# Kernel tuning notes

Measured on AMD Instinct MI355X. Metric: run time of the kernel, lower is better.

## Reference

```python
import jax, jax.numpy as jnp
import numpy as np

NUM_HEADS = 8
SCALE = 0.125  # 1/sqrt(head_dim=64)
NEG_INF = -1e30
LN_EPS = 1e-5


def _layer_norm(x, gamma, beta):
    m = jnp.mean(x, axis=-1, keepdims=True)
    v = jnp.mean(jnp.square(x - m), axis=-1, keepdims=True)
    return (x - m) * jax.lax.rsqrt(v + LN_EPS) * gamma + beta


def setup_inputs() -> dict:
    key = jax.random.key(0)
    ks = jax.random.split(key, 12)
    B, Q, K, D = 2, 2048, 2048, 512
    inp = {
        "query": jax.random.normal(ks[0], (B, Q, D), jnp.float32),
        "key": jax.random.normal(ks[1], (B, K, D), jnp.float32),
        "value": jax.random.normal(ks[2], (B, K, D), jnp.float32),
        "weight_q": jax.random.normal(ks[3], (D, D), jnp.float32) * (1.0 / np.sqrt(D)),
        "weight_k": jax.random.normal(ks[4], (D, D), jnp.float32) * (1.0 / np.sqrt(D)),
        "weight_v": jax.random.normal(ks[5], (D, D), jnp.float32) * (1.0 / np.sqrt(D)),
        "weight_o": jax.random.normal(ks[6], (D, D), jnp.float32) * (1.0 / np.sqrt(D)),
        "g_w": jax.random.normal(ks[7], (2 * D, D), jnp.float32) * (1.0 / np.sqrt(2 * D)),
        "g_b": jnp.ones((D,), jnp.float32),  # g_net bias init to 1.0
        "q_gamma": jnp.ones((D,), jnp.float32),
        "q_beta": jnp.zeros((D,), jnp.float32),
        "k_gamma": jnp.ones((D,), jnp.float32),
        "k_beta": jnp.zeros((D,), jnp.float32),
        "v_gamma": jnp.ones((D,), jnp.float32),
        "v_beta": jnp.zeros((D,), jnp.float32),
        "query_mask": jax.random.randint(ks[8], (B, Q), 0, 2, jnp.int32),
        "key_mask": jax.random.randint(ks[9], (B, K), 0, 2, jnp.int32),
    }
    return inp


def reference(query, key, value, weight_q, weight_k, weight_v, weight_o,
              g_w, g_b, q_gamma, q_beta, k_gamma, k_beta, v_gamma, v_beta,
              query_mask, key_mask):
    B, Q, D = query.shape
    H = NUM_HEADS
    original_query = query

    # add_zero_attn: append an all-zero key/value slot (mask bit = 1)
    key = jnp.concatenate([key, jnp.zeros((B, 1, key.shape[-1]), key.dtype)], axis=1)
    value = jnp.concatenate([value, jnp.zeros((B, 1, value.shape[-1]), value.dtype)], axis=1)
    km = jnp.concatenate([key_mask, jnp.ones((B, 1), key_mask.dtype)], axis=1)
    Kp = key.shape[1]  # klen + 1

    # pre_lnorm
    qn = _layer_norm(query, q_gamma, q_beta)
    kn = _layer_norm(key, k_gamma, k_beta)
    vn = _layer_norm(value, v_gamma, v_beta)

    # multi-head dot-product scores: [B, Q, Kp, H]
    qh = (qn @ weight_q).reshape(B, Q, H, -1)
    kh = (kn @ weight_k).reshape(B, Kp, H, -1)
    score = jnp.einsum('bind,bjnd->bijn', qh, kh) * SCALE
    score = jnp.where(km[:, None, :, None] == 0, NEG_INF, score)
    attn = jax.nn.softmax(score, axis=2)  # softmax over klen (dim=2)

    # weighted values
    vh = (vn @ weight_v).reshape(B, Kp, H, -1)
    attn_vec = jnp.einsum('bijn,bjnd->bind', attn, vh).reshape(B, Q, -1)

    # query mask zeroing
    attn_vec = jnp.where(query_mask[:, :, None] == 0, jnp.zeros((), attn_vec.dtype), attn_vec)

    # output projection
    attn_vec = attn_vec @ weight_o

    # gated combination
    g = jax.nn.sigmoid(jnp.concatenate([original_query, attn_vec], axis=-1) @ g_w + g_b)
    attn_out = g * original_query + (1.0 - g) * attn_vec

    # residual
    attn_out = original_query + attn_out
    return attn_out
```

## Files before the change

kernel.cpp:

```cpp
#include <hip/hip_runtime.h>

typedef float f32x4 __attribute__((ext_vector_type(4)));
typedef short s16x8 __attribute__((ext_vector_type(8)));

#define DEV __device__ __forceinline__

DEV short f2bf(float f) {
    union { float f; unsigned u; } v; v.f = f;
    unsigned r = v.u + 0x7fffu + ((v.u >> 16) & 1u);
    return (short)(r >> 16);
}
DEV float bf2f(short s) {
    union { unsigned u; float f; } v; v.u = ((unsigned)(unsigned short)s) << 16;
    return v.f;
}

#define SEQ    2048
#define DMODEL 512
#define KPAD   2080
#define NROWS  32768

#define OFF_QN   0ull
#define OFF_KN   4194304ull
#define OFF_VN   8519680ull
#define OFF_QH   12845056ull
#define OFF_KH   17039360ull
#define OFF_VH   21364736ull
#define OFF_VHT  25690112ull
#define OFF_AV   29949952ull
#define OFF_WQT  34144256ull
#define WS_NEEDED 37289984ull
#define OFF_ON   0ull
#define OFF_ML   21364736ull
#define OFF_KB   29949952ull
#define OFF_AP   17039360ull

__global__ __launch_bounds__(256) void ln_all(
    const float* __restrict__ q, const float* __restrict__ k, const float* __restrict__ v,
    const float* __restrict__ qg, const float* __restrict__ qb,
    const float* __restrict__ kg, const float* __restrict__ kb2,
    const float* __restrict__ vg, const float* __restrict__ vb,
    short* __restrict__ qn, short* __restrict__ kn, short* __restrict__ vn)
{
    int bid = blockIdx.x;
    const float *in, *gamma, *beta; short* out; int Sreal, Spad;
    if (bid < 1024)      { in=q; gamma=qg; beta=qb;  out=qn; Sreal=SEQ; Spad=SEQ;  }
    else if (bid < 2080) { bid-=1024; in=k; gamma=kg; beta=kb2; out=kn; Sreal=SEQ; Spad=KPAD; }
    else                 { bid-=2080; in=v; gamma=vg; beta=vb;  out=vn; Sreal=SEQ; Spad=KPAD; }

    int w = threadIdx.x >> 6, l = threadIdx.x & 63;
    int r = bid * 4 + w;
    short* op = out + (size_t)r * DMODEL + l * 8;
    s16x8 o = {0,0,0,0,0,0,0,0};
    if (r >= 2 * Spad) { *(s16x8*)op = o; return; }
    int b = r / Spad, j = r - b * Spad;
    if (j >= Sreal) {
        if (j == Sreal) {
            f32x4 b0 = *(const f32x4*)(beta + l*8);
            f32x4 b1 = *(const f32x4*)(beta + l*8 + 4);
            #pragma unroll
            for (int t=0;t<4;t++){ o[t]=f2bf(b0[t]); o[t+4]=f2bf(b1[t]); }
        }
        *(s16x8*)op = o; return;
    }
    const float* ip = in + ((size_t)b * Sreal + j) * DMODEL + l * 8;
    f32x4 x0 = *(const f32x4*)ip;
    f32x4 x1 = *(const f32x4*)(ip + 4);
    float s = x0[0]+x0[1]+x0[2]+x0[3]+x1[0]+x1[1]+x1[2]+x1[3];
    #pragma unroll
    for (int off=1; off<64; off<<=1) s += __shfl_xor(s, off);
    float mean = s * (1.0f/512.0f);
    float vs = 0.f;
    #pragma unroll
    for (int t=0;t<4;t++){ float d0=x0[t]-mean, d1=x1[t]-mean; vs += d0*d0 + d1*d1; }
    #pragma unroll
    for (int off=1; off<64; off<<=1) vs += __shfl_xor(vs, off);
    float rstd = rsqrtf(vs * (1.0f/512.0f) + 1e-5f);
    f32x4 g0 = *(const f32x4*)(gamma + l*8), g1 = *(const f32x4*)(gamma + l*8 + 4);
    f32x4 b0 = *(const f32x4*)(beta + l*8),  b1 = *(const f32x4*)(beta + l*8 + 4);
    #pragma unroll
    for (int t=0;t<4;t++){
        o[t]   = f2bf((x0[t]-mean)*rstd*g0[t] + b0[t]);
        o[t+4] = f2bf((x1[t]-mean)*rstd*g1[t] + b1[t]);
    }
    *(s16x8*)op = o;
}

__global__ __launch_bounds__(256) void wt_all(
    const float* __restrict__ Wq, const float* __restrict__ Wk,
    const float* __restrict__ Wv, const float* __restrict__ Wo,
    const float* __restrict__ gW, short* __restrict__ WT,
    const int* __restrict__ km, float* __restrict__ kbias)
{
    int bid = blockIdx.x;
    if (bid >= 1536) {
        int i = (bid - 1536) * 256 + threadIdx.x;
        if (i >= 2 * KPAD) return;
        int b = i / KPAD, j = i - b * KPAD;
        float v;
        if (j < SEQ)       v = km[b*SEQ + j] ? 0.0f : -1e30f;
        else if (j == SEQ) v = 0.0f;
        else               v = -1e30f;
        kbias[i] = v;
        return;
    }
    const float* in; short* out; int K;
    if (bid < 1024) {
        int wsel = bid >> 8;
        in = (wsel==0) ? Wq : (wsel==1) ? Wk : (wsel==2) ? Wv : Wo;
        out = WT + (size_t)wsel * 262144;
        K = 512; bid &= 255;
    } else {
        in = gW; out = WT + 1048576; K = 1024; bid -= 1024;
    }
    __shared__ float t[32][33];
    int bx = bid & 15, by = bid >> 4;
    int n0 = bx * 32, k0 = by * 32;
    int tx = threadIdx.x & 31, ty = threadIdx.x >> 5;
    #pragma unroll
    for (int i=0;i<4;i++)
        t[ty + i*8][tx] = in[(size_t)(k0 + ty + i*8) * 512 + n0 + tx];
    __syncthreads();
    #pragma unroll
    for (int i=0;i<4;i++)
        out[(size_t)(n0 + ty + i*8) * K + k0 + tx] = f2bf(t[tx][ty + i*8]);
}

template<int MODE, int KK>
__global__ __launch_bounds__(256) void gemm_u(
    const short* __restrict__ A, const float* __restrict__ F1, const float* __restrict__ F2,
    const short* __restrict__ WT,
    short* __restrict__ O0, short* __restrict__ O1, short* __restrict__ O2,
    float* __restrict__ FO, const float* __restrict__ bias)
{
    __shared__ short As[128*64];
    __shared__ short Bs[64*64];
    int tid = threadIdx.x;
    int w = tid >> 6, l = tid & 63;
    int lr = l & 15, lg = l >> 4;
    int tn = blockIdx.x & 7, tm = blockIdx.x >> 3;
    int srow = tid >> 3, sslot = tid & 7;

    const short* Bseg = WT;
    if (MODE == 0) {
        int seg = (tm < 32) ? 0 : (tm < 65) ? 1 : 2;
        Bseg = WT + (size_t)seg * 262144;
    }

    f32x4 acc[2][4];
    #pragma unroll
    for (int m=0;m<2;m++)
        #pragma unroll
        for (int n=0;n<4;n++) acc[m][n] = (f32x4){0.f,0.f,0.f,0.f};

    for (int k0 = 0; k0 < KK; k0 += 64) {
        #pragma unroll
        for (int i=0;i<2;i++){
            int row = i*32 + srow;
            int gslot = sslot ^ (row & 7);
            const short* gb = Bseg + (size_t)(tn*64 + row) * KK + k0 + gslot*8;
            short* lb = Bs + (i*256 + w*64) * 8;
            __builtin_amdgcn_global_load_lds((const __attribute__((address_space(1))) void*)gb,
                                             (__attribute__((address_space(3))) void*)lb, 16, 0, 0);
        }
        if (MODE != 2) {
            #pragma unroll
            for (int i=0;i<4;i++){
                int row = i*32 + srow;
                int gslot = sslot ^ (row & 7);
                const short* ga = A + (size_t)(tm*128 + row) * KK + k0 + gslot*8;
                short* la = As + (i*256 + w*64) * 8;
                __builtin_amdgcn_global_load_lds((const __attribute__((address_space(1))) void*)ga,
                                                 (__attribute__((address_space(3))) void*)la, 16, 0, 0);
            }
        } else {
            const float* src = (k0 < 512) ? F1 : F2;
            int csub = (k0 < 512) ? k0 : k0 - 512;
            #pragma unroll
            for (int i=0;i<4;i++){
                int row = i*32 + srow;
                const float* gp = src + (size_t)(tm*128 + row) * 512 + csub + sslot*8;
                f32x4 a0 = *(const f32x4*)gp;
                f32x4 a1 = *(const f32x4*)(gp + 4);
                s16x8 o;
                #pragma unroll
                for (int t=0;t<4;t++){ o[t] = f2bf(a0[t]); o[t+4] = f2bf(a1[t]); }
                *(s16x8*)(As + row*64 + (sslot ^ (row & 7))*8) = o;
            }
        }
        __syncthreads();
        #pragma unroll
        for (int s=0;s<2;s++){
            s16x8 af[2], bfr[4];
            #pragma unroll
            for (int m=0;m<2;m++){
                int row = w*32 + m*16 + lr;
                int slot = (s*4 + lg) ^ (row & 7);
                af[m] = *(const s16x8*)(As + row*64 + slot*8);
            }
            #pragma unroll
            for (int n=0;n<4;n++){
                int row = n*16 + lr;
                int slot = (s*4 + lg) ^ (row & 7);
                bfr[n] = *(const s16x8*)(Bs + row*64 + slot*8);
            }
            #pragma unroll
            for (int m=0;m<2;m++)
                #pragma unroll
                for (int n=0;n<4;n++)
                    acc[m][n] = __builtin_amdgcn_mfma_f32_16x16x32_bf16(af[m], bfr[n], acc[m][n], 0, 0, 0);
        }
        __syncthreads();
    }

    #pragma unroll
    for (int n=0;n<4;n++){
        int col = tn*64 + n*16 + lr;
        float badd = (MODE == 2) ? bias[col] : 0.0f;
        #pragma unroll
        for (int m=0;m<2;m++){
            #pragma unroll
            for (int j=0;j<4;j++){
                int row = tm*128 + w*32 + m*16 + lg*4 + j;
                float v = acc[m][n][j];
                if (MODE == 0) {
                    short bv = f2bf(v);
                    if (row < 4096) {
                        O0[(size_t)row*512 + col] = bv;
                    } else if (row < 8320) {
                        int r2 = row - 4096;
                        if (r2 < 4160) O1[(size_t)r2*512 + col] = bv;
                    } else {
                        int r2 = row - 8320;
                        if (r2 < 4160) O2[(size_t)r2*512 + col] = bv;
                    }
                } else if (MODE == 1) {
                    FO[(size_t)row*512 + col] = v;
                } else {
                    size_t idx = (size_t)row*512 + col;
                    float g = 1.0f / (1.0f + __expf(-(v + badd)));
                    float q = F1[idx], a = F2[idx];
                    FO[idx] = q + g*q + (1.0f - g)*a;
                }
            }
        }
    }
}

__global__ __launch_bounds__(256) void transpose_v(
    const short* __restrict__ vh, short* __restrict__ vhT)
{
    __shared__ short t[64][72];
    int tid = threadIdx.x, bid = blockIdx.x;
    int kt = bid % 33; int hh = (bid / 33) & 7; int b = bid / (33*8);
    int k0 = kt * 64;
    int rr = tid >> 3, c8 = (tid & 7) * 8;
    #pragma unroll
    for (int p=0;p<2;p++){
        int kr = p*32 + rr;
        int gk = k0 + kr;
        s16x8 v = {0,0,0,0,0,0,0,0};
        if (gk < KPAD) v = *(const s16x8*)(vh + (size_t)(b*KPAD + gk)*DMODEL + hh*64 + c8);
        *(s16x8*)&t[kr][c8] = v;
    }
    __syncthreads();
    #pragma unroll
    for (int p=0;p<2;p++){
        int dr = p*32 + rr;
        if (k0 + c8 < KPAD){
            s16x8 o;
            #pragma unroll
            for (int j2=0;j2<8;j2++) o[j2] = t[c8+j2][dr];
            *(s16x8*)(vhT + ((size_t)(b*8 + hh)*64 + dr)*KPAD + k0 + c8) = o;
        }
    }
}

__global__ __launch_bounds__(256, 6) void flash_kernel(
    const short* __restrict__ qh, const short* __restrict__ kh,
    const short* __restrict__ vhT, const float* __restrict__ kbias,
    short* __restrict__ On, float* __restrict__ ml)
{
    __shared__ short Ks[64*64];
    __shared__ short Vs[64*64];
    __shared__ short plds[4][16*72];
    int tid = threadIdx.x;
    int w = tid >> 6, l = tid & 63;
    int bid = blockIdx.x;
    int h = bid & 7;
    int b = (bid >> 3) & 1;
    int t = bid >> 4;
    int qblk = t / 3;
    int split = t - qblk * 3;
    int q0 = qblk * 64 + w * 16;
    int cl = l & 15, rg = l >> 4;
    int srow = tid >> 3, sslot = tid & 7;

    const short* qp = qh + ((size_t)(b*SEQ + q0 + cl))*DMODEL + h*64 + rg*8;
    s16x8 qf0 = *(const s16x8*)qp;
    s16x8 qf1 = *(const s16x8*)(qp + 32);

    f32x4 O[4];
    float mrow[4], lsum[4];
    #pragma unroll
    for (int n=0;n<4;n++) O[n] = (f32x4){0.f,0.f,0.f,0.f};
    #pragma unroll
    for (int j=0;j<4;j++){ mrow[j] = -1e30f; lsum[j] = 0.f; }

    const short* khb = kh + (size_t)b*KPAD*DMODEL + h*64;
    const short* vtb = vhT + (size_t)(b*8 + h)*64*KPAD;
    const float* kbb = kbias + b*KPAD;
    short* pl = plds[w];

    int kc0 = split * 11;
    int kcN = kc0 + ((split == 2) ? 10 : 11);
    for (int kc = kc0; kc < kcN; ++kc) {
        int k0 = kc * 64;
        if (kc > kc0) __syncthreads();
        #pragma unroll
        for (int i=0;i<2;i++){
            int row = i*32 + srow;
            int gslot = sslot ^ (row & 7);
            const short* gk = khb + (size_t)(k0 + row)*DMODEL + gslot*8;
            const short* gv = vtb + (size_t)row*KPAD + k0 + gslot*8;
            short* lk = Ks + (i*256 + w*64)*8;
            short* lv = Vs + (i*256 + w*64)*8;
            __builtin_amdgcn_global_load_lds((const __attribute__((address_space(1))) void*)gk,
                                             (__attribute__((address_space(3))) void*)lk, 16, 0, 0);
            __builtin_amdgcn_global_load_lds((const __attribute__((address_space(1))) void*)gv,
                                             (__attribute__((address_space(3))) void*)lv, 16, 0, 0);
        }
        __syncthreads();

        float sv[4][4];
        #pragma unroll
        for (int nh=0; nh<4; ++nh) {
            int row = nh*16 + cl;
            s16x8 ka  = *(const s16x8*)(Ks + row*64 + ((rg)     ^ (row & 7))*8);
            s16x8 kb2 = *(const s16x8*)(Ks + row*64 + ((4 + rg) ^ (row & 7))*8);
            f32x4 z = (f32x4){0.f,0.f,0.f,0.f};
            z = __builtin_amdgcn_mfma_f32_16x16x32_bf16(qf0, ka,  z, 0, 0, 0);
            z = __builtin_amdgcn_mfma_f32_16x16x32_bf16(qf1, kb2, z, 0, 0, 0);
            float bias = kbb[k0 + nh*16 + cl];
            #pragma unroll
            for (int j=0;j<4;j++) sv[nh][j] = fmaf(z[j], 0.125f, bias);
        }
        float ml4[4];
        #pragma unroll
        for (int j=0;j<4;j++)
            ml4[j] = fmaxf(fmaxf(sv[0][j], sv[1][j]), fmaxf(sv[2][j], sv[3][j]));
        #pragma unroll
        for (int off=1; off<16; off<<=1){
            #pragma unroll
            for (int j=0;j<4;j++) ml4[j] = fmaxf(ml4[j], __shfl_xor(ml4[j], off));
        }
        bool need = (ml4[0] > mrow[0]+8.f) || (ml4[1] > mrow[1]+8.f) ||
                    (ml4[2] > mrow[2]+8.f) || (ml4[3] > mrow[3]+8.f);
        if (__any(need)) {
            #pragma unroll
            for (int j=0;j<4;j++){
                float mn = fmaxf(mrow[j], ml4[j]);
                float sc = __expf(mrow[j] - mn);
                mrow[j] = mn; lsum[j] *= sc;
                #pragma unroll
                for (int n=0;n<4;n++) O[n][j] *= sc;
            }
        }
        float ps[4] = {0.f,0.f,0.f,0.f};
        #pragma unroll
        for (int nh=0; nh<4; ++nh){
            #pragma unroll
            for (int j=0;j<4;j++){
                float p = __expf(sv[nh][j] - mrow[j]);
                ps[j] += p;
                pl[(rg*4 + j)*72 + nh*16 + cl] = f2bf(p);
            }
        }
        #pragma unroll
        for (int off=1; off<16; off<<=1){
            #pragma unroll
            for (int j=0;j<4;j++) ps[j] += __shfl_xor(ps[j], off);
        }
        #pragma unroll
        for (int j=0;j<4;j++) lsum[j] += ps[j];

        s16x8 pa0 = *(const s16x8*)(pl + cl*72 + rg*8);
        s16x8 pa1 = *(const s16x8*)(pl + cl*72 + 32 + rg*8);
        __builtin_amdgcn_s_setprio(1);
        #pragma unroll
        for (int n=0;n<4;n++){
            int row = n*16 + cl;
            s16x8 vf0 = *(const s16x8*)(Vs + row*64 + ((rg)     ^ (row & 7))*8);
            s16x8 vf1 = *(const s16x8*)(Vs + row*64 + ((4 + rg) ^ (row & 7))*8);
            O[n] = __builtin_amdgcn_mfma_f32_16x16x32_bf16(pa0, vf0, O[n], 0, 0, 0);
            O[n] = __builtin_amdgcn_mfma_f32_16x16x32_bf16(pa1, vf1, O[n], 0, 0, 0);
        }
        __builtin_amdgcn_s_setprio(0);
    }

    if (split == 2) {
        int k0 = 2048;
        float sv[2][4];
        #pragma unroll
        for (int nh=0; nh<2; ++nh) {
            const short* kp = khb + (size_t)(k0 + nh*16 + cl)*DMODEL + rg*8;
            s16x8 ka = *(const s16x8*)kp;
            s16x8 kb2 = *(const s16x8*)(kp + 32);
            f32x4 z = (f32x4){0.f,0.f,0.f,0.f};
            z = __builtin_amdgcn_mfma_f32_16x16x32_bf16(qf0, ka,  z, 0, 0, 0);
            z = __builtin_amdgcn_mfma_f32_16x16x32_bf16(qf1, kb2, z, 0, 0, 0);
            float bias = kbb[k0 + nh*16 + cl];
            #pragma unroll
            for (int j=0;j<4;j++) sv[nh][j] = fmaf(z[j], 0.125f, bias);
        }
        float ml4[4];
        #pragma unroll
        for (int j=0;j<4;j++) ml4[j] = fmaxf(sv[0][j], sv[1][j]);
        #pragma unroll
        for (int off=1; off<16; off<<=1){
            #pragma unroll
            for (int j=0;j<4;j++) ml4[j] = fmaxf(ml4[j], __shfl_xor(ml4[j], off));
        }
        bool need = (ml4[0] > mrow[0]+8.f) || (ml4[1] > mrow[1]+8.f) ||
                    (ml4[2] > mrow[2]+8.f) || (ml4[3] > mrow[3]+8.f);
        if (__any(need)) {
            #pragma unroll
            for (int j=0;j<4;j++){
                float mn = fmaxf(mrow[j], ml4[j]);
                float sc = __expf(mrow[j] - mn);
                mrow[j] = mn; lsum[j] *= sc;
                #pragma unroll
                for (int n=0;n<4;n++) O[n][j] *= sc;
            }
        }
        float ps[4] = {0.f,0.f,0.f,0.f};
        #pragma unroll
        for (int nh=0; nh<2; ++nh){
            #pragma unroll
            for (int j=0;j<4;j++){
                float p = __expf(sv[nh][j] - mrow[j]);
                ps[j] += p;
                pl[(rg*4 + j)*72 + nh*16 + cl] = f2bf(p);
            }
        }
        #pragma unroll
        for (int off=1; off<16; off<<=1){
            #pragma unroll
            for (int j=0;j<4;j++) ps[j] += __shfl_xor(ps[j], off);
        }
        #pragma unroll
        for (int j=0;j<4;j++) lsum[j] += ps[j];

        s16x8 pa0 = *(const s16x8*)(pl + cl*72 + rg*8);
        __builtin_amdgcn_s_setprio(1);
        #pragma unroll
        for (int n=0;n<4;n++){
            s16x8 vf0 = *(const s16x8*)(vtb + (size_t)(n*16 + cl)*KPAD + k0 + rg*8);
            O[n] = __builtin_amdgcn_mfma_f32_16x16x32_bf16(pa0, vf0, O[n], 0, 0, 0);
        }
        __builtin_amdgcn_s_setprio(0);
    }

    int rbase = ((b*8 + h) << 11) + q0;
    #pragma unroll
    for (int j=0;j<4;j++){
        int r = rbase + rg*4 + j;
        float invl = 1.0f / lsum[j];
        #pragma unroll
        for (int n=0;n<4;n++)
            On[((size_t)split*NROWS + r)*64 + n*16 + cl] = f2bf(O[n][j] * invl);
        if (cl == 0){
            ml[((size_t)split*NROWS + r)*2    ] = mrow[j];
            ml[((size_t)split*NROWS + r)*2 + 1] = lsum[j];
        }
    }
}

__global__ __launch_bounds__(256) void merge_kernel(
    const short* __restrict__ On, const float* __restrict__ ml,
    const int* __restrict__ qmask, short* __restrict__ av)
{
    int tid = threadIdx.x;
    int r = blockIdx.x * 32 + (tid >> 3);
    int d8 = (tid & 7) * 8;
    float m0 = ml[(size_t)r*2],              l0 = ml[(size_t)r*2 + 1];
    float m1 = ml[((size_t)NROWS + r)*2],    l1 = ml[((size_t)NROWS + r)*2 + 1];
    float m2 = ml[((size_t)2*NROWS + r)*2],  l2 = ml[((size_t)2*NROWS + r)*2 + 1];
    float m = fmaxf(m0, fmaxf(m1, m2));
    float w0 = l0 * __expf(m0 - m), w1 = l1 * __expf(m1 - m), w2 = l2 * __expf(m2 - m);
    int qrow = r & 2047, bh = r >> 11, h = bh & 7, b = bh >> 3;
    int qm = qmask[b*SEQ + qrow];
    float inv = qm ? 1.0f / (w0 + w1 + w2) : 0.0f;
    w0 *= inv; w1 *= inv; w2 *= inv;
    s16x8 o0 = *(const s16x8*)(On + (size_t)r*64 + d8);
    s16x8 o1 = *(const s16x8*)(On + ((size_t)NROWS + r)*64 + d8);
    s16x8 o2 = *(const s16x8*)(On + ((size_t)2*NROWS + r)*64 + d8);
    s16x8 o;
    #pragma unroll
    for (int e=0;e<8;e++) o[e] = f2bf(w0*bf2f(o0[e]) + w1*bf2f(o1[e]) + w2*bf2f(o2[e]));
    *(s16x8*)(av + ((size_t)(b*SEQ + qrow))*DMODEL + h*64 + d8) = o;
}

extern "C" void kernel_launch(void* const* d_in, const int* in_sizes, int n_in,
                              void* d_out, int out_size, void* d_ws, size_t ws_size,
                              hipStream_t stream)
{
    const float* query = (const float*)d_in[0];
    const float* key   = (const float*)d_in[1];
    const float* value = (const float*)d_in[2];
    const float* Wq    = (const float*)d_in[3];
    const float* Wk    = (const float*)d_in[4];
    const float* Wv    = (const float*)d_in[5];
    const float* Wo    = (const float*)d_in[6];
    const float* gW    = (const float*)d_in[7];
    const float* gB    = (const float*)d_in[8];
    const float* qg    = (const float*)d_in[9];
    const float* qb    = (const float*)d_in[10];
    const float* kg    = (const float*)d_in[11];
    const float* kb    = (const float*)d_in[12];
    const float* vg    = (const float*)d_in[13];
    const float* vb    = (const float*)d_in[14];
    const int* qmask   = (const int*)d_in[15];
    const int* kmask   = (const int*)d_in[16];
    float* out = (float*)d_out;
    char* ws = (char*)d_ws;

    if (ws_size < WS_NEEDED) return;

    short* qn  = (short*)(ws + OFF_QN);
    short* kn  = (short*)(ws + OFF_KN);
    short* vn  = (short*)(ws + OFF_VN);
    short* qh  = (short*)(ws + OFF_QH);
    short* khp = (short*)(ws + OFF_KH);
    short* vhp = (short*)(ws + OFF_VH);
    short* vhT = (short*)(ws + OFF_VHT);
    short* av  = (short*)(ws + OFF_AV);
    short* WT  = (short*)(ws + OFF_WQT);
    short* WoT = WT + 3*262144;
    short* gWT = WT + 1048576;
    short* On  = (short*)(ws + OFF_ON);
    float* mlp = (float*)(ws + OFF_ML);
    float* kbp = (float*)(ws + OFF_KB);
    float* ap  = (float*)(ws + OFF_AP);

    ln_all<<<3136, 256, 0, stream>>>(query, key, value, qg, qb, kg, kb, vg, vb, qn, kn, vn);

    wt_all<<<1553, 256, 0, stream>>>(Wq, Wk, Wv, Wo, gW, WT, kmask, kbp);

    gemm_u<0,512><<<784, 256, 0, stream>>>(qn, nullptr, nullptr, WT, qh, khp, vhp, nullptr, nullptr);

    transpose_v<<<528, 256, 0, stream>>>(vhp, vhT);

    flash_kernel<<<1536, 256, 0, stream>>>(qh, khp, vhT, kbp, On, mlp);
    merge_kernel<<<1024, 256, 0, stream>>>(On, mlp, qmask, av);

    gemm_u<1,512><<<256, 256, 0, stream>>>(av, nullptr, nullptr, WoT, nullptr, nullptr, nullptr, ap, nullptr);

    gemm_u<2,1024><<<256, 256, 0, stream>>>(nullptr, query, ap, gWT, nullptr, nullptr, nullptr, out, gB);

    (void)in_sizes; (void)n_in; (void)out_size;
}
```

Measured before the change: 240.2 us.

## Fuse prep kernels, fold split-merge into output GEMM, shrink GEMM tiles to 64x64

The layernorm and weight-transpose/key-bias kernels are merged into one launch, and padding rows shrink (KPAD rows trimmed to 2064 blocks). The split-K flash merge is folded into the Wo GEMM's A-tile loader, which drops a kernel launch and the intermediate av buffer round-trip. GEMM tiles go from 128x64 to 64x64 with a 2x2 wave layout, doubling the grid for better CU occupancy. The cost is recomputing the merge weights per k-block in the GEMM and smaller MFMA reuse per block.

Result: faster. 231.4 us (-3.7%).

```diff
diff --git a/kernel.cpp b/kernel.cpp
--- a/kernel.cpp
+++ b/kernel.cpp
@@ -22,86 +22,83 @@
 
 #define OFF_QN   0ull
 #define OFF_KN   4194304ull
-#define OFF_VN   8519680ull
+#define OFF_VN   8454144ull
 #define OFF_QH   12845056ull
 #define OFF_KH   17039360ull
 #define OFF_VH   21364736ull
 #define OFF_VHT  25690112ull
-#define OFF_AV   29949952ull
+#define OFF_KB   29949952ull
+#define OFF_ML   29966592ull
 #define OFF_WQT  34144256ull
 #define WS_NEEDED 37289984ull
 #define OFF_ON   0ull
-#define OFF_ML   21364736ull
-#define OFF_KB   29949952ull
 #define OFF_AP   17039360ull
 
-__global__ __launch_bounds__(256) void ln_all(
+__global__ __launch_bounds__(256) void prep_all(
     const float* __restrict__ q, const float* __restrict__ k, const float* __restrict__ v,
     const float* __restrict__ qg, const float* __restrict__ qb,
     const float* __restrict__ kg, const float* __restrict__ kb2,
     const float* __restrict__ vg, const float* __restrict__ vb,
-    short* __restrict__ qn, short* __restrict__ kn, short* __restrict__ vn)
+    const float* __restrict__ Wq, const float* __restrict__ Wk,
+    const float* __restrict__ Wv, const float* __restrict__ Wo,
+    const float* __restrict__ gW, const int* __restrict__ km,
+    short* __restrict__ qn, short* __restrict__ kn, short* __restrict__ vn,
+    short* __restrict__ WT, float* __restrict__ kbias)
 {
     int bid = blockIdx.x;
-    const float *in, *gamma, *beta; short* out; int Sreal, Spad;
-    if (bid < 1024)      { in=q; gamma=qg; beta=qb;  out=qn; Sreal=SEQ; Spad=SEQ;  }
-    else if (bid < 2080) { bid-=1024; in=k; gamma=kg; beta=kb2; out=kn; Sreal=SEQ; Spad=KPAD; }
-    else                 { bid-=2080; in=v; gamma=vg; beta=vb;  out=vn; Sreal=SEQ; Spad=KPAD; }
-
-    int w = threadIdx.x >> 6, l = threadIdx.x & 63;
-    int r = bid * 4 + w;
-    short* op = out + (size_t)r * DMODEL + l * 8;
-    s16x8 o = {0,0,0,0,0,0,0,0};
-    if (r >= 2 * Spad) { *(s16x8*)op = o; return; }
-    int b = r / Spad, j = r - b * Spad;
-    if (j >= Sreal) {
-        if (j == Sreal) {
-            f32x4 b0 = *(const f32x4*)(beta + l*8);
-            f32x4 b1 = *(const f32x4*)(beta + l*8 + 4);
-            #pragma unroll
-            for (int t=0;t<4;t++){ o[t]=f2bf(b0[t]); o[t+4]=f2bf(b1[t]); }
-        }
-        *(s16x8*)op = o; return;
-    }
-    const float* ip = in + ((size_t)b * Sreal + j) * DMODEL + l * 8;
-    f32x4 x0 = *(const f32x4*)ip;
-    f32x4 x1 = *(const f32x4*)(ip + 4);
-    float s = x0[0]+x0[1]+x0[2]+x0[3]+x1[0]+x1[1]+x1[2]+x1[3];
-    #pragma unroll
-    for (int off=1; off<64; off<<=1) s += __shfl_xor(s, off);
-    float mean = s * (1.0f/512.0f);
-    float vs = 0.f;
-    #pragma unroll
-    for (int t=0;t<4;t++){ float d0=x0[t]-mean, d1=x1[t]-mean; vs += d0*d0 + d1*d1; }
-    #pragma unroll
-    for (int off=1; off<64; off<<=1) vs += __shfl_xor(vs, off);
-    float rstd = rsqrtf(vs * (1.0f/512.0f) + 1e-5f);
-    f32x4 g0 = *(const f32x4*)(gamma + l*8), g1 = *(const f32x4*)(gamma + l*8 + 4);
-    f32x4 b0 = *(const f32x4*)(beta + l*8),  b1 = *(const f32x4*)(beta + l*8 + 4);
-    #pragma unroll
-    for (int t=0;t<4;t++){
-        o[t]   = f2bf((x0[t]-mean)*rstd*g0[t] + b0[t]);
-        o[t+4] = f2bf((x1[t]-mean)*rstd*g1[t] + b1[t]);
-    }
-    *(s16x8*)op = o;
-}
-
-__global__ __launch_bounds__(256) void wt_all(
-    const float* __restrict__ Wq, const float* __restrict__ Wk,
-    const float* __restrict__ Wv, const float* __restrict__ Wo,
-    const float* __restrict__ gW, short* __restrict__ WT,
-    const int* __restrict__ km, float* __restrict__ kbias)
-{
-    int bid = blockIdx.x;
+    if (bid < 3104) {
+        const float *in, *gamma, *beta; short* out; int Spad;
+        if (bid < 1024)      { in=q; gamma=qg; beta=qb;  out=qn; Spad=SEQ;  }
+        else if (bid < 2064) { bid-=1024; in=k; gamma=kg; beta=kb2; out=kn; Spad=KPAD; }
+        else                 { bid-=2064; in=v; gamma=vg; beta=vb;  out=vn; Spad=KPAD; }
+
+        int w = threadIdx.x >> 6, l = threadIdx.x & 63;
+        int r = bid * 4 + w;
+        short* op = out + (size_t)r * DMODEL + l * 8;
+        s16x8 o = {0,0,0,0,0,0,0,0};
+        int b = r / Spad, j = r - b * Spad;
+        if (j >= SEQ) {
+            if (j == SEQ) {
+                f32x4 b0 = *(const f32x4*)(beta + l*8);
+                f32x4 b1 = *(const f32x4*)(beta + l*8 + 4);
+                #pragma unroll
+                for (int t=0;t<4;t++){ o[t]=f2bf(b0[t]); o[t+4]=f2bf(b1[t]); }
+            }
+            *(s16x8*)op = o; return;
+        }
+        const float* ip = in + ((size_t)b * SEQ + j) * DMODEL + l * 8;
+        f32x4 x0 = *(const f32x4*)ip;
+        f32x4 x1 = *(const f32x4*)(ip + 4);
+        float s = x0[0]+x0[1]+x0[2]+x0[3]+x1[0]+x1[1]+x1[2]+x1[3];
+        #pragma unroll
+        for (int off=1; off<64; off<<=1) s += __shfl_xor(s, off);
+        float mean = s * (1.0f/512.0f);
+        float vs = 0.f;
+        #pragma unroll
+        for (int t=0;t<4;t++){ float d0=x0[t]-mean, d1=x1[t]-mean; vs += d0*d0 + d1*d1; }
+        #pragma unroll
+        for (int off=1; off<64; off<<=1) vs += __shfl_xor(vs, off);
+        float rstd = rsqrtf(vs * (1.0f/512.0f) + 1e-5f);
+        f32x4 g0 = *(const f32x4*)(gamma + l*8), g1 = *(const f32x4*)(gamma + l*8 + 4);
+        f32x4 b0 = *(const f32x4*)(beta + l*8),  b1 = *(const f32x4*)(beta + l*8 + 4);
+        #pragma unroll
+        for (int t=0;t<4;t++){
+            o[t]   = f2bf((x0[t]-mean)*rstd*g0[t] + b0[t]);
+            o[t+4] = f2bf((x1[t]-mean)*rstd*g1[t] + b1[t]);
+        }
+        *(s16x8*)op = o;
+        return;
+    }
+    bid -= 3104;
     if (bid >= 1536) {
         int i = (bid - 1536) * 256 + threadIdx.x;
         if (i >= 2 * KPAD) return;
         int b = i / KPAD, j = i - b * KPAD;
-        float v;
-        if (j < SEQ)       v = km[b*SEQ + j] ? 0.0f : -1e30f;
-        else if (j == SEQ) v = 0.0f;
-        else               v = -1e30f;
-        kbias[i] = v;
+        float val;
+        if (j < SEQ)       val = km[b*SEQ + j] ? 0.0f : -1e30f;
+        else if (j == SEQ) val = 0.0f;
+        else               val = -1e30f;
+        kbias[i] = val;
         return;
     }
     const float* in; short* out; int K;
@@ -127,31 +124,33 @@
 }
 
 template<int MODE, int KK>
-__global__ __launch_bounds__(256) void gemm_u(
+__global__ __launch_bounds__(256) void gemm64(
     const short* __restrict__ A, const float* __restrict__ F1, const float* __restrict__ F2,
     const short* __restrict__ WT,
     short* __restrict__ O0, short* __restrict__ O1, short* __restrict__ O2,
-    float* __restrict__ FO, const float* __restrict__ bias)
+    float* __restrict__ FO, const float* __restrict__ bias,
+    const short* __restrict__ On, const float* __restrict__ mlp, const int* __restrict__ qmask)
 {
-    __shared__ short As[128*64];
+    __shared__ short As[64*64];
     __shared__ short Bs[64*64];
     int tid = threadIdx.x;
     int w = tid >> 6, l = tid & 63;
     int lr = l & 15, lg = l >> 4;
-    int tn = blockIdx.x & 7, tm = blockIdx.x >> 3;
+    int tm = blockIdx.x >> 3, tn = blockIdx.x & 7;
+    int wm = w >> 1, wn = w & 1;
     int srow = tid >> 3, sslot = tid & 7;
 
     const short* Bseg = WT;
     if (MODE == 0) {
-        int seg = (tm < 32) ? 0 : (tm < 65) ? 1 : 2;
+        int seg = (tm < 64) ? 0 : (tm < 129) ? 1 : 2;
         Bseg = WT + (size_t)seg * 262144;
     }
 
-    f32x4 acc[2][4];
+    f32x4 acc[2][2];
     #pragma unroll
     for (int m=0;m<2;m++)
         #pragma unroll
-        for (int n=0;n<4;n++) acc[m][n] = (f32x4){0.f,0.f,0.f,0.f};
+        for (int n=0;n<2;n++) acc[m][n] = (f32x4){0.f,0.f,0.f,0.f};
 
     for (int k0 = 0; k0 < KK; k0 += 64) {
         #pragma unroll
@@ -163,23 +162,46 @@
             __builtin_amdgcn_global_load_lds((const __attribute__((address_space(1))) void*)gb,
                                              (__attribute__((address_space(3))) void*)lb, 16, 0, 0);
         }
-        if (MODE != 2) {
-            #pragma unroll
-            for (int i=0;i<4;i++){
+        if (MODE == 0) {
+            #pragma unroll
+            for (int i=0;i<2;i++){
                 int row = i*32 + srow;
                 int gslot = sslot ^ (row & 7);
-                const short* ga = A + (size_t)(tm*128 + row) * KK + k0 + gslot*8;
+                const short* ga = A + (size_t)(tm*64 + row) * KK + k0 + gslot*8;
                 short* la = As + (i*256 + w*64) * 8;
                 __builtin_amdgcn_global_load_lds((const __attribute__((address_space(1))) void*)ga,
                                                  (__attribute__((address_space(3))) void*)la, 16, 0, 0);
             }
+        } else if (MODE == 1) {
+            int h = k0 >> 6;
+            #pragma unroll
+            for (int i=0;i<2;i++){
+                int row = i*32 + srow;
+                int r = tm*64 + row;
+                int b = r >> 11, qrow = r & 2047;
+                int rr = ((b*8 + h) << 11) + qrow;
+                float m0 = mlp[(size_t)rr*2],               l0 = mlp[(size_t)rr*2 + 1];
+                float m1 = mlp[((size_t)NROWS + rr)*2],     l1 = mlp[((size_t)NROWS + rr)*2 + 1];
+                float m2 = mlp[((size_t)2*NROWS + rr)*2],   l2 = mlp[((size_t)2*NROWS + rr)*2 + 1];
+                float mm = fmaxf(m0, fmaxf(m1, m2));
+                float w0 = l0 * __expf(m0 - mm), w1 = l1 * __expf(m1 - mm), w2 = l2 * __expf(m2 - mm);
+                float inv = qmask[b*SEQ + qrow] ? 1.0f / (w0 + w1 + w2) : 0.0f;
+                w0 *= inv; w1 *= inv; w2 *= inv;
+                s16x8 o0 = *(const s16x8*)(On + ((size_t)rr)*64 + sslot*8);
+                s16x8 o1 = *(const s16x8*)(On + ((size_t)NROWS + rr)*64 + sslot*8);
+                s16x8 o2 = *(const s16x8*)(On + ((size_t)2*NROWS + rr)*64 + sslot*8);
+                s16x8 om;
+                #pragma unroll
+                for (int e=0;e<8;e++) om[e] = f2bf(w0*bf2f(o0[e]) + w1*bf2f(o1[e]) + w2*bf2f(o2[e]));
+                *(s16x8*)(As + row*64 + (sslot ^ (row & 7))*8) = om;
+            }
         } else {
             const float* src = (k0 < 512) ? F1 : F2;
             int csub = (k0 < 512) ? k0 : k0 - 512;
             #pragma unroll
-            for (int i=0;i<4;i++){
+            for (int i=0;i<2;i++){
                 int row = i*32 + srow;
-                const float* gp = src + (size_t)(tm*128 + row) * 512 + csub + sslot*8;
+                const float* gp = src + (size_t)(tm*64 + row) * 512 + csub + sslot*8;
                 f32x4 a0 = *(const f32x4*)gp;
                 f32x4 a1 = *(const f32x4*)(gp + 4);
                 s16x8 o;
@@ -191,56 +213,50 @@
         __syncthreads();
         #pragma unroll
         for (int s=0;s<2;s++){
-            s16x8 af[2], bfr[4];
+            s16x8 af[2], bfr[2];
             #pragma unroll
             for (int m=0;m<2;m++){
-                int row = w*32 + m*16 + lr;
+                int row = wm*32 + m*16 + lr;
                 int slot = (s*4 + lg) ^ (row & 7);
                 af[m] = *(const s16x8*)(As + row*64 + slot*8);
             }
             #pragma unroll
-            for (int n=0;n<4;n++){
-                int row = n*16 + lr;
+            for (int n=0;n<2;n++){
+                int row = wn*32 + n*16 + lr;
                 int slot = (s*4 + lg) ^ (row & 7);
                 bfr[n] = *(const s16x8*)(Bs + row*64 + slot*8);
             }
             #pragma unroll
             for (int m=0;m<2;m++)
                 #pragma unroll
-                for (int n=0;n<4;n++)
+                for (int n=0;n<2;n++)
                     acc[m][n] = __builtin_amdgcn_mfma_f32_16x16x32_bf16(af[m], bfr[n], acc[m][n], 0, 0, 0);
         }
         __syncthreads();
     }
 
     #pragma unroll
-    for (int n=0;n<4;n++){
-        int col = tn*64 + n*16 + lr;
+    for (int n=0;n<2;n++){
+        int col = tn*64 + wn*32 + n*16 + lr;
         float badd = (MODE == 2) ? bias[col] : 0.0f;
         #pragma unroll
         for (int m=0;m<2;m++){
             #pragma unroll
             for (int j=0;j<4;j++){
-                int row = tm*128 + w*32 + m*16 + lg*4 + j;
+                int row = tm*64 + wm*32 + m*16 + lg*4 + j;
                 float v = acc[m][n][j];
                 if (MODE == 0) {
                     short bv = f2bf(v);
-                    if (row < 4096) {
-                        O0[(size_t)row*512 + col] = bv;
-                    } else if (row < 8320) {
-                        int r2 = row - 4096;
-                        if (r2 < 4160) O1[(size_t)r2*512 + col] = bv;
-                    } else {
-                        int r2 = row - 8320;
-                        if (r2 < 4160) O2[(size_t)r2*512 + col] = bv;
-                    }
+                    if (row < 4096)      O0[(size_t)row*512 + col] = bv;
+                    else if (row < 8256) O1[(size_t)(row - 4096)*512 + col] = bv;
+                    else                 O2[(size_t)(row - 8256)*512 + col] = bv;
                 } else if (MODE == 1) {
                     FO[(size_t)row*512 + col] = v;
                 } else {
                     size_t idx = (size_t)row*512 + col;
                     float g = 1.0f / (1.0f + __expf(-(v + badd)));
-                    float q = F1[idx], a = F2[idx];
-                    FO[idx] = q + g*q + (1.0f - g)*a;
+                    float qv = F1[idx], a = F2[idx];
+                    FO[idx] = qv + g*qv + (1.0f - g)*a;
                 }
             }
         }
@@ -474,31 +490,6 @@
             ml[((size_t)split*NROWS + r)*2 + 1] = lsum[j];
         }
     }
-}
-
-__global__ __launch_bounds__(256) void merge_kernel(
-    const short* __restrict__ On, const float* __restrict__ ml,
-    const int* __restrict__ qmask, short* __restrict__ av)
-{
-    int tid = threadIdx.x;
-    int r = blockIdx.x * 32 + (tid >> 3);
-    int d8 = (tid & 7) * 8;
-    float m0 = ml[(size_t)r*2],              l0 = ml[(size_t)r*2 + 1];
-    float m1 = ml[((size_t)NROWS + r)*2],    l1 = ml[((size_t)NROWS + r)*2 + 1];
-    float m2 = ml[((size_t)2*NROWS + r)*2],  l2 = ml[((size_t)2*NROWS + r)*2 + 1];
-    float m = fmaxf(m0, fmaxf(m1, m2));
-    float w0 = l0 * __expf(m0 - m), w1 = l1 * __expf(m1 - m), w2 = l2 * __expf(m2 - m);
-    int qrow = r & 2047, bh = r >> 11, h = bh & 7, b = bh >> 3;
-    int qm = qmask[b*SEQ + qrow];
-    float inv = qm ? 1.0f / (w0 + w1 + w2) : 0.0f;
-    w0 *= inv; w1 *= inv; w2 *= inv;
-    s16x8 o0 = *(const s16x8*)(On + (size_t)r*64 + d8);
-    s16x8 o1 = *(const s16x8*)(On + ((size_t)NROWS + r)*64 + d8);
-    s16x8 o2 = *(const s16x8*)(On + ((size_t)2*NROWS + r)*64 + d8);
-    s16x8 o;
-    #pragma unroll
-    for (int e=0;e<8;e++) o[e] = f2bf(w0*bf2f(o0[e]) + w1*bf2f(o1[e]) + w2*bf2f(o2[e]));
-    *(s16x8*)(av + ((size_t)(b*SEQ + qrow))*DMODEL + h*64 + d8) = o;
 }
 
 extern "C" void kernel_launch(void* const* d_in, const int* in_sizes, int n_in,
@@ -534,7 +525,6 @@
     short* khp = (short*)(ws + OFF_KH);
     short* vhp = (short*)(ws + OFF_VH);
     short* vhT = (short*)(ws + OFF_VHT);
-    short* av  = (short*)(ws + OFF_AV);
     short* WT  = (short*)(ws + OFF_WQT);
     short* WoT = WT + 3*262144;
     short* gWT = WT + 1048576;
@@ -543,20 +533,22 @@
     float* kbp = (float*)(ws + OFF_KB);
     float* ap  = (float*)(ws + OFF_AP);
 
-    ln_all<<<3136, 256, 0, stream>>>(query, key, value, qg, qb, kg, kb, vg, vb, qn, kn, vn);
-
-    wt_all<<<1553, 256, 0, stream>>>(Wq, Wk, Wv, Wo, gW, WT, kmask, kbp);
-
-    gemm_u<0,512><<<784, 256, 0, stream>>>(qn, nullptr, nullptr, WT, qh, khp, vhp, nullptr, nullptr);
+    prep_all<<<4657, 256, 0, stream>>>(query, key, value, qg, qb, kg, kb, vg, vb,
+                                       Wq, Wk, Wv, Wo, gW, kmask,
+                                       qn, kn, vn, WT, kbp);
+
+    gemm64<0,512><<<1552, 256, 0, stream>>>(qn, nullptr, nullptr, WT, qh, khp, vhp,
+                                            nullptr, nullptr, nullptr, nullptr, nullptr);
 
     transpose_v<<<528, 256, 0, stream>>>(vhp, vhT);
 
     flash_kernel<<<1536, 256, 0, stream>>>(qh, khp, vhT, kbp, On, mlp);
-    merge_kernel<<<1024, 256, 0, stream>>>(On, mlp, qmask, av);
-
-    gemm_u<1,512><<<256, 256, 0, stream>>>(av, nullptr, nullptr, WoT, nullptr, nullptr, nullptr, ap, nullptr);
-
-    gemm_u<2,1024><<<256, 256, 0, stream>>>(nullptr, query, ap, gWT, nullptr, nullptr, nullptr, out, gB);
+
+    gemm64<1,512><<<512, 256, 0, stream>>>(nullptr, nullptr, nullptr, WoT, nullptr, nullptr, nullptr,
+                                           ap, nullptr, On, mlp, qmask);
+
+    gemm64<2,1024><<<512, 256, 0, stream>>>(nullptr, query, ap, gWT, nullptr, nullptr, nullptr,
+                                            out, gB, nullptr, nullptr, nullptr);
 
     (void)in_sizes; (void)n_in; (void)out_size;
 }
```

## Merge prep kernels, use 128x128 tiles for QKV GEMM and 64x64 for output GEMMs

Applied to the files above, without the earlier changes.

Combines the layer-norm and weight-transpose/key-bias kernels into a single prep launch, removing one kernel launch. The QKV projection gets a dedicated kernel with 128x128 tiles and a 2x2 wave layout, which halves the block count and raises operand reuse per block. The output and gate GEMMs switch to 64x64 tiles with 512 blocks, giving more parallelism on the small M=4096 problems. The trade-off is fewer blocks and more accumulator registers in the QKV kernel, and less data reuse per block in the output GEMMs.

New measurement: 223.0 us. 7.2% less time.

```diff
diff --git a/kernel.cpp b/kernel.cpp
--- a/kernel.cpp
+++ b/kernel.cpp
@@ -35,73 +35,72 @@
 #define OFF_KB   29949952ull
 #define OFF_AP   17039360ull
 
-__global__ __launch_bounds__(256) void ln_all(
+__global__ __launch_bounds__(256) void prep_all(
     const float* __restrict__ q, const float* __restrict__ k, const float* __restrict__ v,
     const float* __restrict__ qg, const float* __restrict__ qb,
     const float* __restrict__ kg, const float* __restrict__ kb2,
     const float* __restrict__ vg, const float* __restrict__ vb,
-    short* __restrict__ qn, short* __restrict__ kn, short* __restrict__ vn)
+    const float* __restrict__ Wq, const float* __restrict__ Wk,
+    const float* __restrict__ Wv, const float* __restrict__ Wo,
+    const float* __restrict__ gW, const int* __restrict__ km,
+    short* __restrict__ qn, short* __restrict__ kn, short* __restrict__ vn,
+    short* __restrict__ WT, float* __restrict__ kbias)
 {
     int bid = blockIdx.x;
-    const float *in, *gamma, *beta; short* out; int Sreal, Spad;
-    if (bid < 1024)      { in=q; gamma=qg; beta=qb;  out=qn; Sreal=SEQ; Spad=SEQ;  }
-    else if (bid < 2080) { bid-=1024; in=k; gamma=kg; beta=kb2; out=kn; Sreal=SEQ; Spad=KPAD; }
-    else                 { bid-=2080; in=v; gamma=vg; beta=vb;  out=vn; Sreal=SEQ; Spad=KPAD; }
-
-    int w = threadIdx.x >> 6, l = threadIdx.x & 63;
-    int r = bid * 4 + w;
-    short* op = out + (size_t)r * DMODEL + l * 8;
-    s16x8 o = {0,0,0,0,0,0,0,0};
-    if (r >= 2 * Spad) { *(s16x8*)op = o; return; }
-    int b = r / Spad, j = r - b * Spad;
-    if (j >= Sreal) {
-        if (j == Sreal) {
-            f32x4 b0 = *(const f32x4*)(beta + l*8);
-            f32x4 b1 = *(const f32x4*)(beta + l*8 + 4);
-            #pragma unroll
-            for (int t=0;t<4;t++){ o[t]=f2bf(b0[t]); o[t+4]=f2bf(b1[t]); }
-        }
-        *(s16x8*)op = o; return;
-    }
-    const float* ip = in + ((size_t)b * Sreal + j) * DMODEL + l * 8;
-    f32x4 x0 = *(const f32x4*)ip;
-    f32x4 x1 = *(const f32x4*)(ip + 4);
-    float s = x0[0]+x0[1]+x0[2]+x0[3]+x1[0]+x1[1]+x1[2]+x1[3];
-    #pragma unroll
-    for (int off=1; off<64; off<<=1) s += __shfl_xor(s, off);
-    float mean = s * (1.0f/512.0f);
-    float vs = 0.f;
-    #pragma unroll
-    for (int t=0;t<4;t++){ float d0=x0[t]-mean, d1=x1[t]-mean; vs += d0*d0 + d1*d1; }
-    #pragma unroll
-    for (int off=1; off<64; off<<=1) vs += __shfl_xor(vs, off);
-    float rstd = rsqrtf(vs * (1.0f/512.0f) + 1e-5f);
-    f32x4 g0 = *(const f32x4*)(gamma + l*8), g1 = *(const f32x4*)(gamma + l*8 + 4);
-    f32x4 b0 = *(const f32x4*)(beta + l*8),  b1 = *(const f32x4*)(beta + l*8 + 4);
-    #pragma unroll
-    for (int t=0;t<4;t++){
-        o[t]   = f2bf((x0[t]-mean)*rstd*g0[t] + b0[t]);
-        o[t+4] = f2bf((x1[t]-mean)*rstd*g1[t] + b1[t]);
-    }
-    *(s16x8*)op = o;
-}
-
-__global__ __launch_bounds__(256) void wt_all(
-    const float* __restrict__ Wq, const float* __restrict__ Wk,
-    const float* __restrict__ Wv, const float* __restrict__ Wo,
-    const float* __restrict__ gW, short* __restrict__ WT,
-    const int* __restrict__ km, float* __restrict__ kbias)
-{
-    int bid = blockIdx.x;
+    if (bid < 3136) {
+        const float *in, *gamma, *beta; short* out; int Spad;
+        if (bid < 1024)      { in=q; gamma=qg; beta=qb;  out=qn; Spad=SEQ;  }
+        else if (bid < 2080) { bid-=1024; in=k; gamma=kg; beta=kb2; out=kn; Spad=KPAD; }
+        else                 { bid-=2080; in=v; gamma=vg; beta=vb;  out=vn; Spad=KPAD; }
+
+        int w = threadIdx.x >> 6, l = threadIdx.x & 63;
+        int r = bid * 4 + w;
+        short* op = out + (size_t)r * DMODEL + l * 8;
+        s16x8 o = {0,0,0,0,0,0,0,0};
+        if (r >= 2 * Spad) { *(s16x8*)op = o; return; }
+        int b = r / Spad, j = r - b * Spad;
+        if (j >= SEQ) {
+            if (j == SEQ) {
+                f32x4 b0 = *(const f32x4*)(beta + l*8);
+                f32x4 b1 = *(const f32x4*)(beta + l*8 + 4);
+                #pragma unroll
+                for (int t=0;t<4;t++){ o[t]=f2bf(b0[t]); o[t+4]=f2bf(b1[t]); }
+            }
+            *(s16x8*)op = o; return;
+        }
+        const float* ip = in + ((size_t)b * SEQ + j) * DMODEL + l * 8;
+        f32x4 x0 = *(const f32x4*)ip;
+        f32x4 x1 = *(const f32x4*)(ip + 4);
+        float s = x0[0]+x0[1]+x0[2]+x0[3]+x1[0]+x1[1]+x1[2]+x1[3];
+        #pragma unroll
+        for (int off=1; off<64; off<<=1) s += __shfl_xor(s, off);
+        float mean = s * (1.0f/512.0f);
+        float vs = 0.f;
+        #pragma unroll
+        for (int t=0;t<4;t++){ float d0=x0[t]-mean, d1=x1[t]-mean; vs += d0*d0 + d1*d1; }
+        #pragma unroll
+        for (int off=1; off<64; off<<=1) vs += __shfl_xor(vs, off);
+        float rstd = rsqrtf(vs * (1.0f/512.0f) + 1e-5f);
+        f32x4 g0 = *(const f32x4*)(gamma + l*8), g1 = *(const f32x4*)(gamma + l*8 + 4);
+        f32x4 b0 = *(const f32x4*)(beta + l*8),  b1 = *(const f32x4*)(beta + l*8 + 4);
+        #pragma unroll
+        for (int t=0;t<4;t++){
+            o[t]   = f2bf((x0[t]-mean)*rstd*g0[t] + b0[t]);
+            o[t+4] = f2bf((x1[t]-mean)*rstd*g1[t] + b1[t]);
+        }
+        *(s16x8*)op = o;
+        return;
+    }
+    bid -= 3136;
     if (bid >= 1536) {
         int i = (bid - 1536) * 256 + threadIdx.x;
         if (i >= 2 * KPAD) return;
         int b = i / KPAD, j = i - b * KPAD;
-        float v;
-        if (j < SEQ)       v = km[b*SEQ + j] ? 0.0f : -1e30f;
-        else if (j == SEQ) v = 0.0f;
-        else               v = -1e30f;
-        kbias[i] = v;
+        float val;
+        if (j < SEQ)       val = km[b*SEQ + j] ? 0.0f : -1e30f;
+        else if (j == SEQ) val = 0.0f;
+        else               val = -1e30f;
+        kbias[i] = val;
         return;
     }
     const float* in; short* out; int K;
@@ -126,49 +125,128 @@
         out[(size_t)(n0 + ty + i*8) * K + k0 + tx] = f2bf(t[tx][ty + i*8]);
 }
 
+__global__ __launch_bounds__(256) void gemm128_qkv(
+    const short* __restrict__ A, const short* __restrict__ WT,
+    short* __restrict__ qh, short* __restrict__ khp, short* __restrict__ vhp)
+{
+    __shared__ short As[128*64];
+    __shared__ short Bs[128*64];
+    int tid = threadIdx.x;
+    int w = tid >> 6, l = tid & 63;
+    int lr = l & 15, lg = l >> 4;
+    int tm = blockIdx.x >> 2, tn = blockIdx.x & 3;
+    int seg = (tm < 32) ? 0 : (tm < 65) ? 1 : 2;
+    const short* Bt = WT + (size_t)seg * 262144;
+    int wm = w >> 1, wn = w & 1;
+    int srow = tid >> 3, sslot = tid & 7;
+
+    f32x4 acc[4][4];
+    #pragma unroll
+    for (int m=0;m<4;m++)
+        #pragma unroll
+        for (int n=0;n<4;n++) acc[m][n] = (f32x4){0.f,0.f,0.f,0.f};
+
+    for (int k0 = 0; k0 < 512; k0 += 64) {
+        #pragma unroll
+        for (int i=0;i<4;i++){
+            int row = i*32 + srow;
+            int gslot = sslot ^ (row & 7);
+            const short* ga = A  + (size_t)(tm*128 + row) * 512 + k0 + gslot*8;
+            const short* gb = Bt + (size_t)(tn*128 + row) * 512 + k0 + gslot*8;
+            short* la = As + (i*32 + w*8) * 64;
+            short* lb = Bs + (i*32 + w*8) * 64;
+            __builtin_amdgcn_global_load_lds((const __attribute__((address_space(1))) void*)ga,
+                                             (__attribute__((address_space(3))) void*)la, 16, 0, 0);
+            __builtin_amdgcn_global_load_lds((const __attribute__((address_space(1))) void*)gb,
+                                             (__attribute__((address_space(3))) void*)lb, 16, 0, 0);
+        }
+        __syncthreads();
+        #pragma unroll
+        for (int s=0;s<2;s++){
+            s16x8 af[4], bfr[4];
+            #pragma unroll
+            for (int m=0;m<4;m++){
+                int row = wm*64 + m*16 + lr;
+                int slot = (s*4 + lg) ^ (row & 7);
+                af[m] = *(const s16x8*)(As + row*64 + slot*8);
+            }
+            #pragma unroll
+            for (int n=0;n<4;n++){
+                int row = wn*64 + n*16 + lr;
+                int slot = (s*4 + lg) ^ (row & 7);
+                bfr[n] = *(const s16x8*)(Bs + row*64 + slot*8);
+            }
+            #pragma unroll
+            for (int m=0;m<4;m++)
+                #pragma unroll
+                for (int n=0;n<4;n++)
+                    acc[m][n] = __builtin_amdgcn_mfma_f32_16x16x32_bf16(af[m], bfr[n], acc[m][n], 0, 0, 0);
+        }
+        __syncthreads();
+    }
+
+    int rb = tm*128 + wm*64;
+    int cb = tn*128 + wn*64;
+    #pragma unroll
+    for (int n=0;n<4;n++){
+        int col = cb + n*16 + lr;
+        #pragma unroll
+        for (int m=0;m<4;m++){
+            #pragma unroll
+            for (int j=0;j<4;j++){
+                int row = rb + m*16 + lg*4 + j;
+                short bv = f2bf(acc[m][n][j]);
+                if (row < 4096) {
+                    qh[(size_t)row*512 + col] = bv;
+                } else if (row < 8320) {
+                    int r2 = row - 4096;
+                    if (r2 < 4160) khp[(size_t)r2*512 + col] = bv;
+                } else {
+                    int r2 = row - 8320;
+                    if (r2 < 4160) vhp[(size_t)r2*512 + col] = bv;
+                }
+            }
+        }
+    }
+}
+
 template<int MODE, int KK>
-__global__ __launch_bounds__(256) void gemm_u(
+__global__ __launch_bounds__(256) void gemm64(
     const short* __restrict__ A, const float* __restrict__ F1, const float* __restrict__ F2,
     const short* __restrict__ WT,
-    short* __restrict__ O0, short* __restrict__ O1, short* __restrict__ O2,
     float* __restrict__ FO, const float* __restrict__ bias)
 {
-    __shared__ short As[128*64];
+    __shared__ short As[64*64];
     __shared__ short Bs[64*64];
     int tid = threadIdx.x;
     int w = tid >> 6, l = tid & 63;
     int lr = l & 15, lg = l >> 4;
-    int tn = blockIdx.x & 7, tm = blockIdx.x >> 3;
+    int tm = blockIdx.x >> 3, tn = blockIdx.x & 7;
+    int wm = w >> 1, wn = w & 1;
     int srow = tid >> 3, sslot = tid & 7;
 
-    const short* Bseg = WT;
-    if (MODE == 0) {
-        int seg = (tm < 32) ? 0 : (tm < 65) ? 1 : 2;
-        Bseg = WT + (size_t)seg * 262144;
-    }
-
-    f32x4 acc[2][4];
+    f32x4 acc[2][2];
     #pragma unroll
     for (int m=0;m<2;m++)
         #pragma unroll
-        for (int n=0;n<4;n++) acc[m][n] = (f32x4){0.f,0.f,0.f,0.f};
+        for (int n=0;n<2;n++) acc[m][n] = (f32x4){0.f,0.f,0.f,0.f};
 
     for (int k0 = 0; k0 < KK; k0 += 64) {
         #pragma unroll
         for (int i=0;i<2;i++){
             int row = i*32 + srow;
             int gslot = sslot ^ (row & 7);
-            const short* gb = Bseg + (size_t)(tn*64 + row) * KK + k0 + gslot*8;
+            const short* gb = WT + (size_t)(tn*64 + row) * KK + k0 + gslot*8;
             short* lb = Bs + (i*256 + w*64) * 8;
             __builtin_amdgcn_global_load_lds((const __attribute__((address_space(1))) void*)gb,
                                              (__attribute__((address_space(3))) void*)lb, 16, 0, 0);
         }
-        if (MODE != 2) {
-            #pragma unroll
-            for (int i=0;i<4;i++){
+        if (MODE == 1) {
+            #pragma unroll
+            for (int i=0;i<2;i++){
                 int row = i*32 + srow;
                 int gslot = sslot ^ (row & 7);
-                const short* ga = A + (size_t)(tm*128 + row) * KK + k0 + gslot*8;
+                const short* ga = A + (size_t)(tm*64 + row) * KK + k0 + gslot*8;
                 short* la = As + (i*256 + w*64) * 8;
                 __builtin_amdgcn_global_load_lds((const __attribute__((address_space(1))) void*)ga,
                                                  (__attribute__((address_space(3))) void*)la, 16, 0, 0);
@@ -177,9 +255,9 @@
             const float* src = (k0 < 512) ? F1 : F2;
             int csub = (k0 < 512) ? k0 : k0 - 512;
             #pragma unroll
-            for (int i=0;i<4;i++){
+            for (int i=0;i<2;i++){
                 int row = i*32 + srow;
-                const float* gp = src + (size_t)(tm*128 + row) * 512 + csub + sslot*8;
+                const float* gp = src + (size_t)(tm*64 + row) * 512 + csub + sslot*8;
                 f32x4 a0 = *(const f32x4*)gp;
                 f32x4 a1 = *(const f32x4*)(gp + 4);
                 s16x8 o;
@@ -191,56 +269,45 @@
         __syncthreads();
         #pragma unroll
         for (int s=0;s<2;s++){
-            s16x8 af[2], bfr[4];
+            s16x8 af[2], bfr[2];
             #pragma unroll
             for (int m=0;m<2;m++){
-                int row = w*32 + m*16 + lr;
+                int row = wm*32 + m*16 + lr;
                 int slot = (s*4 + lg) ^ (row & 7);
                 af[m] = *(const s16x8*)(As + row*64 + slot*8);
             }
             #pragma unroll
-            for (int n=0;n<4;n++){
-                int row = n*16 + lr;
+            for (int n=0;n<2;n++){
+                int row = wn*32 + n*16 + lr;
                 int slot = (s*4 + lg) ^ (row & 7);
                 bfr[n] = *(const s16x8*)(Bs + row*64 + slot*8);
             }
             #pragma unroll
             for (int m=0;m<2;m++)
                 #pragma unroll
-                for (int n=0;n<4;n++)
+                for (int n=0;n<2;n++)
                     acc[m][n] = __builtin_amdgcn_mfma_f32_16x16x32_bf16(af[m], bfr[n], acc[m][n], 0, 0, 0);
         }
         __syncthreads();
     }
 
     #pragma unroll
-    for (int n=0;n<4;n++){
-        int col = tn*64 + n*16 + lr;
+    for (int n=0;n<2;n++){
+        int col = tn*64 + wn*32 + n*16 + lr;
         float badd = (MODE == 2) ? bias[col] : 0.0f;
         #pragma unroll
         for (int m=0;m<2;m++){
             #pragma unroll
             for (int j=0;j<4;j++){
-                int row = tm*128 + w*32 + m*16 + lg*4 + j;
+                int row = tm*64 + wm*32 + m*16 + lg*4 + j;
                 float v = acc[m][n][j];
-                if (MODE == 0) {
-                    short bv = f2bf(v);
-                    if (row < 4096) {
-                        O0[(size_t)row*512 + col] = bv;
-                    } else if (row < 8320) {
-                        int r2 = row - 4096;
-                        if (r2 < 4160) O1[(size_t)r2*512 + col] = bv;
-                    } else {
-                        int r2 = row - 8320;
-                        if (r2 < 4160) O2[(size_t)r2*512 + col] = bv;
-                    }
-                } else if (MODE == 1) {
+                if (MODE == 1) {
                     FO[(size_t)row*512 + col] = v;
                 } else {
                     size_t idx = (size_t)row*512 + col;
                     float g = 1.0f / (1.0f + __expf(-(v + badd)));
-                    float q = F1[idx], a = F2[idx];
-                    FO[idx] = q + g*q + (1.0f - g)*a;
+                    float qv = F1[idx], a = F2[idx];
+                    FO[idx] = qv + g*qv + (1.0f - g)*a;
                 }
             }
         }
@@ -543,20 +610,21 @@
     float* kbp = (float*)(ws + OFF_KB);
     float* ap  = (float*)(ws + OFF_AP);
 
-    ln_all<<<3136, 256, 0, stream>>>(query, key, value, qg, qb, kg, kb, vg, vb, qn, kn, vn);
-
-    wt_all<<<1553, 256, 0, stream>>>(Wq, Wk, Wv, Wo, gW, WT, kmask, kbp);
-
-    gemm_u<0,512><<<784, 256, 0, stream>>>(qn, nullptr, nullptr, WT, qh, khp, vhp, nullptr, nullptr);
+    prep_all<<<4689, 256, 0, stream>>>(query, key, value, qg, qb, kg, kb, vg, vb,
+                                       Wq, Wk, Wv, Wo, gW, kmask,
+                                       qn, kn, vn, WT, kbp);
+
+    gemm128_qkv<<<392, 256, 0, stream>>>(qn, WT, qh, khp, vhp);
 
     transpose_v<<<528, 256, 0, stream>>>(vhp, vhT);
 
     flash_kernel<<<1536, 256, 0, stream>>>(qh, khp, vhT, kbp, On, mlp);
+
     merge_kernel<<<1024, 256, 0, stream>>>(On, mlp, qmask, av);
 
-    gemm_u<1,512><<<256, 256, 0, stream>>>(av, nullptr, nullptr, WoT, nullptr, nullptr, nullptr, ap, nullptr);
-
-    gemm_u<2,1024><<<256, 256, 0, stream>>>(nullptr, query, ap, gWT, nullptr, nullptr, nullptr, out, gB);
+    gemm64<1,512><<<512, 256, 0, stream>>>(av, nullptr, nullptr, WoT, ap, nullptr);
+
+    gemm64<2,1024><<<512, 256, 0, stream>>>(nullptr, query, ap, gWT, out, gB);
 
     (void)in_sizes; (void)n_in; (void)out_size;
 }
```
